# Kernel optimization log

Hardware: AMD Instinct MI355X
Metric: run time of the kernel (lower is better)

The kernel has to match this reference:

```python
import jax, jax.numpy as jnp
import numpy as np

B, C, H, W = 4, 256, 64, 64
INTER = max(1, C // 8)  # 32


def setup_inputs() -> dict:
    key = jax.random.key(0)
    ks = jax.random.split(key, 8)
    s = 0.02  # conv weight init scale
    return {
        "feat": jax.random.normal(ks[0], (B, C, H, W), jnp.float32),
        "edge": jax.random.normal(ks[1], (B, C, H, W), jnp.float32),
        "wq": jax.random.normal(ks[2], (INTER, C), jnp.float32) * s,
        "bq": jnp.zeros((INTER,), jnp.float32),
        "wk": jax.random.normal(ks[3], (INTER, C), jnp.float32) * s,
        "bk": jnp.zeros((INTER,), jnp.float32),
        "wv": jax.random.normal(ks[4], (C, C), jnp.float32) * s,
        "bv": jnp.zeros((C,), jnp.float32),
    }


def reference(feat, edge, wq, bq, wk, bk, wv, bv):
    b, c, h, w = feat.shape
    n = h * w
    # 1x1 convs as channel matmuls; flatten spatial dims to n = H*W tokens
    q = (jnp.einsum('ic,bchw->bihw', wq, feat) + bq[None, :, None, None]).reshape(b, -1, n)  # [B, inter, N]
    k = (jnp.einsum('ic,bchw->bihw', wk, edge) + bk[None, :, None, None]).reshape(b, -1, n)  # [B, inter, N]
    v = (jnp.einsum('oc,bchw->bohw', wv, edge) + bv[None, :, None, None]).reshape(b, c, n)   # [B, C, N]
    # scores[b, nq, nk] = sum_i q[b,i,nq] * k[b,i,nk]; softmax over nk
    attn = jax.nn.softmax(jnp.einsum('bin,bim->bnm', q, k), axis=-1)  # [B, N, N]
    # out[b,c,nq] = sum_m v[b,c,m] * attn[b,nq,m]
    out = jnp.einsum('bcm,bnm->bcn', v, attn).reshape(b, c, h, w)
    return out + feat
```

## Files before the change

kernel.cpp:

```cpp
#include <hip/hip_runtime.h>
#include <cstddef>

#define BB 4
#define CC 256
#define NN 4096
#define NI 32
#define LOG2E 1.4426950408889634f

typedef __attribute__((ext_vector_type(8))) short bf16x8;
typedef __attribute__((ext_vector_type(16))) float f32x16;
typedef __attribute__((ext_vector_type(4))) float f32x4;
typedef unsigned short ushort_t;
typedef unsigned int uint32;

typedef union { uint32 u[4]; bf16x8 v; } fragU;

__device__ __forceinline__ uint32 f2bf_bits(float f) {
    union { float f; uint32 u; } v; v.f = f;
    return (v.u + 0x7fffu + ((v.u >> 16) & 1u)) >> 16;
}
__device__ __forceinline__ uint32 pack2bf(float a, float b) {
    return f2bf_bits(a) | (f2bf_bits(b) << 16);
}
__device__ __forceinline__ uint32 pack2bf_t(float a, float b) {
    union { float f; uint32 u; } A, B; A.f = a; B.f = b;
    return (B.u & 0xFFFF0000u) | (A.u >> 16);
}

__device__ __forceinline__ size_t vfidx(int b, int n, int c) {
    return ((((size_t)b * (NN / 16) + (n >> 4)) * 2 + ((n >> 3) & 1)) * (CC * 8))
           + (size_t)c * 8 + (n & 7);
}

__global__ __launch_bounds__(256) void wconv_kernel(
    const float* __restrict__ wq, const float* __restrict__ wk,
    const float* __restrict__ wv,
    ushort_t* __restrict__ wqF, ushort_t* __restrict__ wkF,
    ushort_t* __restrict__ wvF)
{
    const int bid = blockIdx.x;
    const int t = threadIdx.x;
    if (bid < 64) {
        const int fi = bid * 256 + t;
        const int o  = fi >> 6;
        const int k4 = (fi & 63) * 4;
        const f32x4 x = *(const f32x4*)&wv[(size_t)o * CC + k4];
        const int kkg = k4 >> 4, hh = (k4 >> 3) & 1, j0 = k4 & 7;
        const int ot = o >> 5, lane = hh * 32 + (o & 31);
        uint2 p; p.x = pack2bf(x[0], x[1]); p.y = pack2bf(x[2], x[3]);
        *(uint2*)&wvF[((size_t)(ot * 16 + kkg) * 64 + lane) * 8 + j0] = p;
    } else {
        const int which = (bid - 64) >> 1;
        const int part  = (bid - 64) & 1;
        const float* src = which ? wk : wq;
        ushort_t* dst = which ? wkF : wqF;
        const float sc = which ? 1.0f : LOG2E;
#pragma unroll
        for (int p = 0; p < 4; ++p) {
            const int fi = part * 1024 + p * 256 + t;
            const int o  = fi >> 6;
            const int k4 = (fi & 63) * 4;
            const f32x4 x = *(const f32x4*)&src[(size_t)o * CC + k4];
            const int kkg = k4 >> 4, hh = (k4 >> 3) & 1, j0 = k4 & 7;
            const int lane = hh * 32 + (o & 31);
            uint2 pr; pr.x = pack2bf(x[0] * sc, x[1] * sc);
            pr.y = pack2bf(x[2] * sc, x[3] * sc);
            *(uint2*)&dst[((size_t)kkg * 64 + lane) * 8 + j0] = pr;
        }
    }
}

__global__ __launch_bounds__(256, 1) void proj_kernel(
    const float* __restrict__ feat, const float* __restrict__ edge,
    const ushort_t* __restrict__ wqF, const ushort_t* __restrict__ wkF,
    const ushort_t* __restrict__ wvF,
    const float* __restrict__ bq, const float* __restrict__ bk,
    const float* __restrict__ bv,
    ushort_t* __restrict__ qT, ushort_t* __restrict__ kT,
    ushort_t* __restrict__ vF)
{
    __shared__ __attribute__((aligned(16))) uint32 sF[4][2][64][4];
    __shared__ __attribute__((aligned(16))) uint32 sE[4][2][64][4];

    const int tid = threadIdx.x;
    const int b = blockIdx.y;
    const int n0 = blockIdx.x * 64;
    const int w = tid >> 6, lane = tid & 63;
    const int col = lane & 31, h = lane >> 5;

    const ushort_t* __restrict__ aQK = ((w < 2) ? wqF : wkF) + (size_t)lane * 8;
    const ushort_t* __restrict__ wvB0 = wvF + ((size_t)((2 * w + 0) * 16) * 64 + lane) * 8;
    const ushort_t* __restrict__ wvB1 = wvF + ((size_t)((2 * w + 1) * 16) * 64 + lane) * 8;
    const uint32* __restrict__ bSrc =
        (w == 0) ? &sF[0][0][lane][0] :
        (w == 1) ? &sF[0][1][lane][0] :
        (w == 2) ? &sE[0][0][lane][0] : &sE[0][1][lane][0];

    f32x16 accV[2][2];
    f32x16 accS;
#pragma unroll
    for (int r = 0; r < 16; ++r) {
        accS[r] = 0.f;
        accV[0][0][r] = 0.f; accV[0][1][r] = 0.f;
        accV[1][0][r] = 0.f; accV[1][1][r] = 0.f;
    }

    f32x4 rF[2][2], rE[2][2];

#pragma unroll
    for (int p = 0; p < 2; ++p) {
        const int pi = p * 256 + tid;
        const int m = pi >> 4, cidx = pi & 15;
        const size_t ga = ((size_t)(b * CC + 2 * m)) * NN + n0 + cidx * 4;
        rF[p][0] = *(const f32x4*)&feat[ga];
        rF[p][1] = *(const f32x4*)&feat[ga + NN];
        rE[p][0] = *(const f32x4*)&edge[ga];
        rE[p][1] = *(const f32x4*)&edge[ga + NN];
    }

    for (int ch = 0; ch < 4; ++ch) {
#pragma unroll
        for (int p = 0; p < 2; ++p) {
            const int pi = p * 256 + tid;
            const int m = pi >> 4, cidx = pi & 15;
            const int kk = m >> 3, hh = (m >> 2) & 1, ju = m & 3;
#pragma unroll
            for (int c = 0; c < 4; ++c) {
                const int cn = cidx * 4 + c;
                const int nt = cn >> 5, cl = cn & 31;
                sF[kk][nt][hh * 32 + cl][ju] = pack2bf(rF[p][0][c], rF[p][1][c]);
                sE[kk][nt][hh * 32 + cl][ju] = pack2bf(rE[p][0][c], rE[p][1][c]);
            }
        }
        __syncthreads();

        if (ch < 3) {
            const int c0 = (ch + 1) * 64;
#pragma unroll
            for (int p = 0; p < 2; ++p) {
                const int pi = p * 256 + tid;
                const int m = pi >> 4, cidx = pi & 15;
                const size_t ga = ((size_t)(b * CC + c0 + 2 * m)) * NN + n0 + cidx * 4;
                rF[p][0] = *(const f32x4*)&feat[ga];
                rF[p][1] = *(const f32x4*)&feat[ga + NN];
                rE[p][0] = *(const f32x4*)&edge[ga];
                rE[p][1] = *(const f32x4*)&edge[ga + NN];
            }
        }

#pragma unroll
        for (int kk = 0; kk < 4; ++kk) {
            const int kkg = ch * 4 + kk;
            const bf16x8 eA0 = *(const bf16x8*)&sE[kk][0][lane][0];
            const bf16x8 eA1 = *(const bf16x8*)&sE[kk][1][lane][0];
            const bf16x8 vB0 = *(const bf16x8*)&wvB0[(size_t)kkg * 512];
            const bf16x8 vB1 = *(const bf16x8*)&wvB1[(size_t)kkg * 512];
            const bf16x8 aS  = *(const bf16x8*)&aQK[(size_t)kkg * 512];
            const bf16x8 bS  = *(const bf16x8*)&bSrc[(size_t)kk * 512];
            accS = __builtin_amdgcn_mfma_f32_32x32x16_bf16(aS, bS, accS, 0, 0, 0);
            accV[0][0] = __builtin_amdgcn_mfma_f32_32x32x16_bf16(eA0, vB0, accV[0][0], 0, 0, 0);
            accV[0][1] = __builtin_amdgcn_mfma_f32_32x32x16_bf16(eA0, vB1, accV[0][1], 0, 0, 0);
            accV[1][0] = __builtin_amdgcn_mfma_f32_32x32x16_bf16(eA1, vB0, accV[1][0], 0, 0, 0);
            accV[1][1] = __builtin_amdgcn_mfma_f32_32x32x16_bf16(eA1, vB1, accV[1][1], 0, 0, 0);
        }
        __syncthreads();
    }

    {
        const float* bias = (w < 2) ? bq : bk;
        const float bsc = (w < 2) ? LOG2E : 1.0f;
        ushort_t* dst = (w < 2) ? qT : kT;
        const int nt = w & 1;
        const size_t base = ((size_t)b * NN + n0 + nt * 32 + col) * NI;
#pragma unroll
        for (int q = 0; q < 4; ++q) {
            const int i0 = 8 * q + 4 * h;
            const float x0 = accS[4 * q + 0] + bias[i0 + 0] * bsc;
            const float x1 = accS[4 * q + 1] + bias[i0 + 1] * bsc;
            const float x2 = accS[4 * q + 2] + bias[i0 + 2] * bsc;
            const float x3 = accS[4 * q + 3] + bias[i0 + 3] * bsc;
            uint2 pr; pr.x = pack2bf(x0, x1); pr.y = pack2bf(x2, x3);
            *(uint2*)&dst[base + i0] = pr;
        }
    }

#pragma unroll
    for (int cti = 0; cti < 2; ++cti) {
        const int o = (2 * w + cti) * 32 + col;
        const float vb = bv[o];
#pragma unroll
        for (int mt = 0; mt < 2; ++mt) {
#pragma unroll
            for (int q = 0; q < 4; ++q) {
                const int nst = n0 + mt * 32 + 8 * q + 4 * h;
                uint2 pr;
                pr.x = pack2bf(accV[mt][cti][4 * q + 0] + vb,
                               accV[mt][cti][4 * q + 1] + vb);
                pr.y = pack2bf(accV[mt][cti][4 * q + 2] + vb,
                               accV[mt][cti][4 * q + 3] + vb);
                *(uint2*)&vF[vfidx(b, nst, o)] = pr;
            }
        }
    }
}

__global__ __launch_bounds__(512, 2) void attn_kernel(
    const ushort_t* __restrict__ qT, const ushort_t* __restrict__ kT,
    const ushort_t* __restrict__ vF, const float* __restrict__ feat,
    float* __restrict__ out)
{
    __shared__ float red[4][64][33];
    __shared__ float lpart[4][2][32];
    __shared__ float linvS[64];

    const int tid  = threadIdx.x;
    const int id   = blockIdx.x;
    const int b    = (id & 7) >> 1;
    const int nq0  = (((id >> 3) << 1) | (id & 1)) * 64;
    const int w    = tid >> 6;
    const int lane = tid & 63;
    const int col  = lane & 31;
    const int h    = lane >> 5;
    const int qs   = w & 1;
    const int kg   = w >> 1;

    bf16x8 bQ0, bQ1;
    {
        const size_t qb = ((size_t)b * NN + nq0 + qs * 32 + col) * NI + h * 8;
        bQ0 = *(const bf16x8*)&qT[qb];
        bQ1 = *(const bf16x8*)&qT[qb + 16];
    }

    f32x16 acc[8];
#pragma unroll
    for (int cs = 0; cs < 8; ++cs)
#pragma unroll
        for (int r = 0; r < 16; ++r) acc[cs][r] = 0.f;

    float lp = 0.f;

    const size_t kTb = (size_t)b * NN * NI;
    const int keybase = kg * 1024;

    for (int strip = 0; strip < 32; ++strip) {
        const int key0 = keybase + strip * 32;

        const size_t kb = kTb + (size_t)(key0 + col) * NI + h * 8;
        const bf16x8 aK0 = *(const bf16x8*)&kT[kb];
        const bf16x8 aK1 = *(const bf16x8*)&kT[kb + 16];

        f32x16 st;
#pragma unroll
        for (int r = 0; r < 16; ++r) st[r] = 0.f;
        st = __builtin_amdgcn_mfma_f32_32x32x16_bf16(aK0, bQ0, st, 0, 0, 0);
        st = __builtin_amdgcn_mfma_f32_32x32x16_bf16(aK1, bQ1, st, 0, 0, 0);

        float p[16]; float sum = 0.f;
#pragma unroll
        for (int r = 0; r < 16; ++r) {
            p[r] = __builtin_amdgcn_exp2f(st[r]);
            sum += p[r];
        }
        lp += sum;

        uint32 pk[8];
#pragma unroll
        for (int j = 0; j < 8; ++j) pk[j] = pack2bf_t(p[2 * j], p[2 * j + 1]);
        uint32 rv[8];
#pragma unroll
        for (int j = 0; j < 8; ++j) rv[j] = __shfl_xor(pk[j], 32, 64);
        fragU F0, F1;
        F0.u[0] = h ? rv[2] : pk[0];
        F0.u[1] = h ? rv[3] : pk[1];
        F0.u[2] = h ? pk[2] : rv[0];
        F0.u[3] = h ? pk[3] : rv[1];
        F1.u[0] = h ? rv[6] : pk[4];
        F1.u[1] = h ? rv[7] : pk[5];
        F1.u[2] = h ? pk[6] : rv[4];
        F1.u[3] = h ? pk[7] : rv[5];

        const size_t vbB = (((size_t)b * (NN / 16) + (key0 >> 4)) * 2 + h) * (CC * 8)
                         + (size_t)col * 8;
#pragma unroll
        for (int cs = 0; cs < 8; ++cs) {
            const bf16x8 v0 = *(const bf16x8*)&vF[vbB + cs * 256];
            const bf16x8 v1 = *(const bf16x8*)&vF[vbB + 4096 + cs * 256];
            acc[cs] = __builtin_amdgcn_mfma_f32_32x32x16_bf16(F0.v, v0, acc[cs], 0, 0, 0);
            acc[cs] = __builtin_amdgcn_mfma_f32_32x32x16_bf16(F1.v, v1, acc[cs], 0, 0, 0);
        }
    }

    lp += __shfl_xor(lp, 32, 64);
    if (h == 0) lpart[kg][qs][col] = lp;
    __syncthreads();
    if (tid < 64) {
        const int s = tid >> 5, q = tid & 31;
        linvS[tid] = 1.0f / (lpart[0][s][q] + lpart[1][s][q]
                           + lpart[2][s][q] + lpart[3][s][q]);
    }
    __syncthreads();

    const int c32 = tid >> 4;
    const int q4  = (tid & 15) * 4;
    float lv[4];
#pragma unroll
    for (int j = 0; j < 4; ++j) lv[j] = linvS[q4 + j];

#pragma unroll
    for (int pp = 0; pp < 8; ++pp) {
#pragma unroll
        for (int r = 0; r < 16; ++r) {
            const int row = qs * 32 + (r & 3) + 8 * (r >> 2) + 4 * h;
            red[kg][row][col] = acc[pp][r];
        }
        __syncthreads();
        {
            const int cglob = pp * 32 + c32;
            const size_t gb = ((size_t)b * CC + cglob) * NN + nq0 + q4;
            float o[4];
#pragma unroll
            for (int j = 0; j < 4; ++j)
                o[j] = red[0][q4 + j][c32] + red[1][q4 + j][c32]
                     + red[2][q4 + j][c32] + red[3][q4 + j][c32];
            const float4 f4 = *(const float4*)&feat[gb];
            float4 o4;
            o4.x = o[0] * lv[0] + f4.x;
            o4.y = o[1] * lv[1] + f4.y;
            o4.z = o[2] * lv[2] + f4.z;
            o4.w = o[3] * lv[3] + f4.w;
            *(float4*)&out[gb] = o4;
        }
        __syncthreads();
    }
}

extern "C" void kernel_launch(void* const* d_in, const int* in_sizes, int n_in,
                              void* d_out, int out_size, void* d_ws, size_t ws_size,
                              hipStream_t stream)
{
    (void)in_sizes; (void)n_in; (void)out_size; (void)ws_size;
    const float* feat = (const float*)d_in[0];
    const float* edge = (const float*)d_in[1];
    const float* wq   = (const float*)d_in[2];
    const float* bq   = (const float*)d_in[3];
    const float* wk   = (const float*)d_in[4];
    const float* bk   = (const float*)d_in[5];
    const float* wv   = (const float*)d_in[6];
    const float* bv   = (const float*)d_in[7];
    float* out = (float*)d_out;

    ushort_t* qT  = (ushort_t*)d_ws;
    ushort_t* kT  = qT + (size_t)BB * NN * NI;
    ushort_t* vF  = kT + (size_t)BB * NN * NI;

    ushort_t* wvF = (ushort_t*)d_out;
    ushort_t* wqF = wvF + (size_t)CC * CC;
    ushort_t* wkF = wqF + (size_t)NI * CC;

    wconv_kernel<<<dim3(68), 256, 0, stream>>>(wq, wk, wv, wqF, wkF, wvF);
    proj_kernel<<<dim3(NN / 64, BB), 256, 0, stream>>>(feat, edge, wqF, wkF, wvF,
                                                       bq, bk, bv, qT, kT, vF);
    attn_kernel<<<dim3(NN / 64 * BB), 512, 0, stream>>>(qT, kT, vF, feat, out);
}
```

Measured before the change: 154.6 us.

## Halve query tile per block and split keys across all eight waves

Each attention block now covers 32 queries instead of 64, and all eight waves split the key range eight ways instead of two query slices times four key groups. The grid doubles to 512 blocks so more than one block can run per CU and wave occupancy rises. In exchange, K/V global reads per query double and the cross-wave LDS reduction now sums eight partials.

Result: slower. 211.2 us (+36.6%).

```diff
diff --git a/kernel.cpp b/kernel.cpp
--- a/kernel.cpp
+++ b/kernel.cpp
@@ -209,24 +209,22 @@
     const ushort_t* __restrict__ vF, const float* __restrict__ feat,
     float* __restrict__ out)
 {
-    __shared__ float red[4][64][33];
-    __shared__ float lpart[4][2][32];
-    __shared__ float linvS[64];
+    __shared__ float red[8][32][33];
+    __shared__ float lpart[8][32];
+    __shared__ float linvS[32];
 
     const int tid  = threadIdx.x;
     const int id   = blockIdx.x;
     const int b    = (id & 7) >> 1;
-    const int nq0  = (((id >> 3) << 1) | (id & 1)) * 64;
+    const int nq0  = (((id >> 3) << 1) | (id & 1)) * 32;
     const int w    = tid >> 6;
     const int lane = tid & 63;
     const int col  = lane & 31;
     const int h    = lane >> 5;
-    const int qs   = w & 1;
-    const int kg   = w >> 1;
 
     bf16x8 bQ0, bQ1;
     {
-        const size_t qb = ((size_t)b * NN + nq0 + qs * 32 + col) * NI + h * 8;
+        const size_t qb = ((size_t)b * NN + nq0 + col) * NI + h * 8;
         bQ0 = *(const bf16x8*)&qT[qb];
         bQ1 = *(const bf16x8*)&qT[qb + 16];
     }
@@ -240,9 +238,9 @@
     float lp = 0.f;
 
     const size_t kTb = (size_t)b * NN * NI;
-    const int keybase = kg * 1024;
-
-    for (int strip = 0; strip < 32; ++strip) {
+    const int keybase = w * 512;
+
+    for (int strip = 0; strip < 16; ++strip) {
         const int key0 = keybase + strip * 32;
 
         const size_t kb = kTb + (size_t)(key0 + col) * NI + h * 8;
@@ -291,44 +289,43 @@
     }
 
     lp += __shfl_xor(lp, 32, 64);
-    if (h == 0) lpart[kg][qs][col] = lp;
+    if (h == 0) lpart[w][col] = lp;
     __syncthreads();
-    if (tid < 64) {
-        const int s = tid >> 5, q = tid & 31;
-        linvS[tid] = 1.0f / (lpart[0][s][q] + lpart[1][s][q]
-                           + lpart[2][s][q] + lpart[3][s][q]);
+    if (tid < 32) {
+        float s = 0.f;
+#pragma unroll
+        for (int g = 0; g < 8; ++g) s += lpart[g][tid];
+        linvS[tid] = 1.0f / s;
     }
     __syncthreads();
 
     const int c32 = tid >> 4;
-    const int q4  = (tid & 15) * 4;
-    float lv[4];
-#pragma unroll
-    for (int j = 0; j < 4; ++j) lv[j] = linvS[q4 + j];
+    const int qp  = (tid & 15) * 2;
+    const float lv0 = linvS[qp];
+    const float lv1 = linvS[qp + 1];
 
 #pragma unroll
     for (int pp = 0; pp < 8; ++pp) {
 #pragma unroll
         for (int r = 0; r < 16; ++r) {
-            const int row = qs * 32 + (r & 3) + 8 * (r >> 2) + 4 * h;
-            red[kg][row][col] = acc[pp][r];
+            const int row = (r & 3) + 8 * (r >> 2) + 4 * h;
+            red[w][row][col] = acc[pp][r];
         }
         __syncthreads();
         {
             const int cglob = pp * 32 + c32;
-            const size_t gb = ((size_t)b * CC + cglob) * NN + nq0 + q4;
-            float o[4];
-#pragma unroll
-            for (int j = 0; j < 4; ++j)
-                o[j] = red[0][q4 + j][c32] + red[1][q4 + j][c32]
-                     + red[2][q4 + j][c32] + red[3][q4 + j][c32];
-            const float4 f4 = *(const float4*)&feat[gb];
-            float4 o4;
-            o4.x = o[0] * lv[0] + f4.x;
-            o4.y = o[1] * lv[1] + f4.y;
-            o4.z = o[2] * lv[2] + f4.z;
-            o4.w = o[3] * lv[3] + f4.w;
-            *(float4*)&out[gb] = o4;
+            const size_t gb = ((size_t)b * CC + cglob) * NN + nq0 + qp;
+            float o0 = 0.f, o1 = 0.f;
+#pragma unroll
+            for (int g = 0; g < 8; ++g) {
+                o0 += red[g][qp][c32];
+                o1 += red[g][qp + 1][c32];
+            }
+            const float2 f2 = *(const float2*)&feat[gb];
+            float2 o2;
+            o2.x = o0 * lv0 + f2.x;
+            o2.y = o1 * lv1 + f2.y;
+            *(float2*)&out[gb] = o2;
         }
         __syncthreads();
     }
@@ -360,5 +357,5 @@
     wconv_kernel<<<dim3(68), 256, 0, stream>>>(wq, wk, wv, wqF, wkF, wvF);
     proj_kernel<<<dim3(NN / 64, BB), 256, 0, stream>>>(feat, edge, wqF, wkF, wvF,
                                                        bq, bk, bv, qT, kT, vF);
-    attn_kernel<<<dim3(NN / 64 * BB), 512, 0, stream>>>(qT, kT, vF, feat, out);
-}
+    attn_kernel<<<dim3(NN / 32 * BB), 512, 0, stream>>>(qT, kT, vF, feat, out);
+}
```
